# Kernel optimization log

Measured on AMD Instinct MI355X. Metric: run time of the kernel, lower is better.

The kernel has to match this reference:

```python
import jax, jax.numpy as jnp
import numpy as np
from jax import lax


def setup_inputs() -> dict:
    key = jax.random.key(0)
    kx, kw = jax.random.split(key)
    x = jax.random.normal(kx, (8, 32, 16, 160, 160), dtype=jnp.float32)
    # xavier-normal-ish init (scale irrelevant to correctness testing)
    weights = jax.random.normal(kw, (32, 32, 1, 3, 3), dtype=jnp.float32) * 0.1
    return {"x": x, "weights": weights}


def reference(x, weights):
    # per-(out_ch, in_ch) scale: mean |w| over kernel dims (2,3,4), detached
    scale = lax.stop_gradient(jnp.mean(jnp.abs(weights), axis=(2, 3, 4), keepdims=True))
    binary_no_grad = scale * jnp.sign(weights)          # {+-scale}
    clipped = jnp.clip(weights, -1.0, 1.0)
    # straight-through estimator: value = binary_no_grad, grad flows via clipped
    binary_weights = lax.stop_gradient(binary_no_grad - clipped) + clipped
    out = lax.conv_general_dilated(
        x, binary_weights,
        window_strides=(1, 1, 1),
        padding=((0, 0), (1, 1), (1, 1)),
        rhs_dilation=(1, 1, 1),
        dimension_numbers=("NCDHW", "OIDHW", "NCDHW"),
        feature_group_count=1,
    )
    return out
```

## Files before the change

kernel.cpp:

```cpp
#include <hip/hip_runtime.h>
#include <stdint.h>


typedef _Float16 half8  __attribute__((ext_vector_type(8)));
typedef float    floatx4 __attribute__((ext_vector_type(4)));

#define DHW 409600
#define HW  25600
#define RING_SLOT_B 10368
#define RING_B      41472
#define SCR_SLOT_B  20480
#define LDS_TOTAL   102912

__device__ __forceinline__ int w1s(int w1) { return w1 ^ ((w1 >> 2) & 1); }
__device__ __forceinline__ int f2v(int w1) { return ((w1 >> 1) ^ (w1 >> 3)) & 3; }

typedef const __attribute__((address_space(1))) uint32_t* gas1;
typedef __attribute__((address_space(3))) uint32_t* las3;
__device__ __forceinline__ void gld16(const void* g, void* l) {
    __builtin_amdgcn_global_load_lds((gas1)g, (las3)l, 16, 0, 0);
}
#define VMCNT(N) do { asm volatile("s_waitcnt vmcnt(" #N ")" ::: "memory"); \
                      __builtin_amdgcn_sched_barrier(0); } while (0)
__device__ __forceinline__ void barrier_raw() {
    __builtin_amdgcn_sched_barrier(0);
    asm volatile("s_waitcnt lgkmcnt(0)" ::: "memory");
    __builtin_amdgcn_s_barrier();
    __builtin_amdgcn_sched_barrier(0);
}

__global__ void bnn_wprep_kernel(const float* __restrict__ w,
                                 _Float16* __restrict__ ws) {
    const int tid = threadIdx.x;
    #pragma unroll
    for (int p4 = 0; p4 < 4; ++p4) {
        const int oi = tid * 4 + p4;
        const int o  = oi >> 5;
        const int i  = oi & 31;
        const float* wp = w + oi * 9;
        float s = 0.f;
        #pragma unroll
        for (int t = 0; t < 9; ++t) s += fabsf(wp[t]);
        s *= (1.f / 9.f);
        const int l = ((i >> 3) << 4) | (o & 15);
        const int p = o >> 4;
        const int j = i & 7;
        #pragma unroll
        for (int t = 0; t < 9; ++t) {
            const float v  = wp[t];
            const float sg = (v > 0.f) ? 1.f : ((v < 0.f) ? -1.f : 0.f);
            ws[((t * 2 + p) * 64 + l) * 8 + j] = (_Float16)(s * sg);
        }
    }
}

__global__ __launch_bounds__(320) void bnn_conv3d_dma(
        const float* __restrict__ x, const _Float16* __restrict__ ws,
        float* __restrict__ out) {
    extern __shared__ __align__(16) char lds[];

    const int tid  = threadIdx.x;
    const int lane = tid & 63;
    const int wv   = tid >> 6;

    const int bid = blockIdx.x;
    const int hc  = bid & 3;
    const int d   = (bid >> 2) & 15;
    const int n   = bid >> 6;
    const int h0  = hc * 40;

    const float* qb[4];
    {
        const int chl = lane >> 3;
        const int wl  = (lane & 7) * 4;
        #pragma unroll
        for (int q = 0; q < 4; ++q)
            qb[q] = x + (size_t)(n * 32 + q * 8 + chl) * DHW + d * HW + wv * 32 + wl;
    }

    half8 wf0[9], wf1[9];
    {
        const half8* fb = (const half8*)ws;
        #pragma unroll
        for (int t = 0; t < 9; ++t) {
            wf0[t] = fb[(t * 2 + 0) * 64 + lane];
            wf1[t] = fb[(t * 2 + 1) * 64 + lane];
        }
    }
    asm volatile("s_waitcnt vmcnt(0)" ::: "memory");
    __builtin_amdgcn_sched_barrier(0);

    if (tid < 128) {
        const int slot = tid >> 5, w1x = ((tid >> 4) & 1) ? 161 : 0, word = tid & 15;
        *(uint32_t*)(lds + slot * RING_SLOT_B + w1x * 64 + word * 4) = 0u;
    }

    const int pcell = 32 * wv + 1 + (lane >> 1);
    const int w1p   = w1s(pcell);
    const int wloc  = (w1p - 1) - wv * 32;
    const int chb   = (lane & 1) * 16;
    int soff[16];
    #pragma unroll
    for (int c = 0; c < 16; ++c) {
        const int ch = chb + c;
        soff[c] = (wv * 4 + (ch >> 3)) * 1024 + ((ch & 7) * 8 + (wloc >> 2)) * 16
                + (wloc & 3) * 4;
    }
    const int f2p = f2v(pcell);
    const int rb0 = pcell * 64 + ((((lane & 1) * 2)     ^ f2p) * 16);
    const int rb1 = pcell * 64 + ((((lane & 1) * 2 + 1) ^ f2p) * 16);

    const int s16 = lane & 15, kgr = lane >> 4;
    int rdo[2][3];
    #pragma unroll
    for (int gi = 0; gi < 2; ++gi)
        #pragma unroll
        for (int kw = 0; kw < 3; ++kw) {
            const int w1 = (2 * wv + gi) * 16 + s16 + kw;
            rdo[gi][kw] = (w1s(w1) * 32 + ((kgr ^ f2v(w1)) * 8)) * 2;
        }
    float* ob = out + (size_t)(n * 32 + s16) * DHW + d * HW + wv * 32 + kgr * 4;

    auto DMA = [&](int r) {
        int h = h0 - 1 + r; h = h < 0 ? 0 : (h > 159 ? 159 : h);
        char* dst = lds + RING_B + (r % 3) * SCR_SLOT_B + wv * 4096;
        #pragma unroll
        for (int q = 0; q < 4; ++q)
            gld16(qb[q] + h * 160, dst + q * 1024);
        __builtin_amdgcn_sched_barrier(0);
    };
    auto PACK = [&](int r) {
        const int hr = h0 - 1 + r;
        const char* sl = lds + RING_B + (r % 3) * SCR_SLOT_B;
        char* rg = lds + (r & 3) * RING_SLOT_B;
        half8 o0 = {}, o1 = {};
        if (hr >= 0 && hr < 160) {
            float f[16];
            #pragma unroll
            for (int c = 0; c < 16; ++c) f[c] = *(const float*)(sl + soff[c]);
            #pragma unroll
            for (int c = 0; c < 8; ++c) { o0[c] = (_Float16)f[c]; o1[c] = (_Float16)f[c + 8]; }
        }
        *(half8*)(rg + rb0) = o0;
        *(half8*)(rg + rb1) = o1;
    };
    auto COMPUTE = [&](int t) {
        #pragma unroll
        for (int gi = 0; gi < 2; ++gi) {
            floatx4 a0 = {0.f, 0.f, 0.f, 0.f};
            floatx4 a1 = {0.f, 0.f, 0.f, 0.f};
            #pragma unroll
            for (int kh = 0; kh < 3; ++kh) {
                const char* sb = lds + ((t + kh) & 3) * RING_SLOT_B;
                #pragma unroll
                for (int kw = 0; kw < 3; ++kw) {
                    const half8 a = *(const half8*)(sb + rdo[gi][kw]);
                    const int tp = kh * 3 + kw;
                    a0 = __builtin_amdgcn_mfma_f32_16x16x32_f16(a, wf0[tp], a0, 0, 0, 0);
                    a1 = __builtin_amdgcn_mfma_f32_16x16x32_f16(a, wf1[tp], a1, 0, 0, 0);
                }
            }
            float* op = ob + (size_t)(h0 + t) * 160 + gi * 16;
            *(floatx4*)op = a0;
            *(floatx4*)(op + (size_t)16 * DHW) = a1;
        }
    };

    DMA(0); DMA(1); DMA(2);
    VMCNT(8);  PACK(0);
    VMCNT(4);  PACK(1);
    barrier_raw();
    DMA(3);
    VMCNT(4);  PACK(2); barrier_raw(); DMA(4); COMPUTE(0);
    VMCNT(8);  PACK(3); barrier_raw(); DMA(5); COMPUTE(1);
    for (int t = 2; t <= 37; ++t) {
        VMCNT(12); PACK(t + 2); barrier_raw(); DMA(t + 4); COMPUTE(t);
    }
    VMCNT(12); PACK(40); barrier_raw(); COMPUTE(38);
    VMCNT(8);  PACK(41); barrier_raw(); COMPUTE(39);
}

extern "C" void kernel_launch(void* const* d_in, const int* in_sizes, int n_in,
                              void* d_out, int out_size, void* d_ws, size_t ws_size,
                              hipStream_t stream) {
    const float* x = (const float*)d_in[0];
    const float* w = (const float*)d_in[1];
    float* out = (float*)d_out;
    _Float16* ws = (_Float16*)d_ws;
    bnn_wprep_kernel<<<dim3(1), dim3(256), 0, stream>>>(w, ws);
    (void)hipFuncSetAttribute((const void*)&bnn_conv3d_dma,
                              hipFuncAttributeMaxDynamicSharedMemorySize, LDS_TOTAL);
    bnn_conv3d_dma<<<dim3(512), dim3(320), LDS_TOTAL, stream>>>(x, ws, out);
}
```

Before: 188.5 us.

## Drop halo columns and triple staging buffer to fit two blocks per CU

Removes the zero-padded halo cells from the fp16 ring, clamping column reads instead and zeroing the A fragment with a select at the image edges. The fp32 staging scratch goes from three slots to two, and the prologue gets an extra barrier to keep the reuse safe. Together these cut dynamic LDS from about 100 KB to 80 KB, so two blocks can share a CU and hide memory latency better. The cost is a couple of extra selects per compute step and a tighter DMA/pack reuse window.

```diff
diff --git a/kernel.cpp b/kernel.cpp
--- a/kernel.cpp
+++ b/kernel.cpp
@@ -7,10 +7,10 @@
 
 #define DHW 409600
 #define HW  25600
-#define RING_SLOT_B 10368
-#define RING_B      41472
+#define RING_SLOT_B 10240
+#define RING_B      40960
 #define SCR_SLOT_B  20480
-#define LDS_TOTAL   102912
+#define LDS_TOTAL   81920
 
 __device__ __forceinline__ int w1s(int w1) { return w1 ^ ((w1 >> 2) & 1); }
 __device__ __forceinline__ int f2v(int w1) { return ((w1 >> 1) ^ (w1 >> 3)) & 3; }
@@ -90,14 +90,9 @@
     asm volatile("s_waitcnt vmcnt(0)" ::: "memory");
     __builtin_amdgcn_sched_barrier(0);
 
-    if (tid < 128) {
-        const int slot = tid >> 5, w1x = ((tid >> 4) & 1) ? 161 : 0, word = tid & 15;
-        *(uint32_t*)(lds + slot * RING_SLOT_B + w1x * 64 + word * 4) = 0u;
-    }
-
-    const int pcell = 32 * wv + 1 + (lane >> 1);
+    const int pcell = 32 * wv + (lane >> 1);
     const int w1p   = w1s(pcell);
-    const int wloc  = (w1p - 1) - wv * 32;
+    const int wloc  = w1p - wv * 32;
     const int chb   = (lane & 1) * 16;
     int soff[16];
     #pragma unroll
@@ -116,14 +111,17 @@
     for (int gi = 0; gi < 2; ++gi)
         #pragma unroll
         for (int kw = 0; kw < 3; ++kw) {
-            const int w1 = (2 * wv + gi) * 16 + s16 + kw;
-            rdo[gi][kw] = (w1s(w1) * 32 + ((kgr ^ f2v(w1)) * 8)) * 2;
+            int wq = (2 * wv + gi) * 16 + s16 + kw - 1;
+            wq = wq < 0 ? 0 : (wq > 159 ? 159 : wq);
+            rdo[gi][kw] = (w1s(wq) * 32 + ((kgr ^ f2v(wq)) * 8)) * 2;
         }
+    const bool okA = (wv * 32 + s16 - 1) >= 0;
+    const bool okB = (wv * 32 + 16 + s16 + 1) < 160;
     float* ob = out + (size_t)(n * 32 + s16) * DHW + d * HW + wv * 32 + kgr * 4;
 
     auto DMA = [&](int r) {
         int h = h0 - 1 + r; h = h < 0 ? 0 : (h > 159 ? 159 : h);
-        char* dst = lds + RING_B + (r % 3) * SCR_SLOT_B + wv * 4096;
+        char* dst = lds + RING_B + (r & 1) * SCR_SLOT_B + wv * 4096;
         #pragma unroll
         for (int q = 0; q < 4; ++q)
             gld16(qb[q] + h * 160, dst + q * 1024);
@@ -131,7 +129,7 @@
     };
     auto PACK = [&](int r) {
         const int hr = h0 - 1 + r;
-        const char* sl = lds + RING_B + (r % 3) * SCR_SLOT_B;
+        const char* sl = lds + RING_B + (r & 1) * SCR_SLOT_B;
         char* rg = lds + (r & 3) * RING_SLOT_B;
         half8 o0 = {}, o1 = {};
         if (hr >= 0 && hr < 160) {
@@ -145,6 +143,7 @@
         *(half8*)(rg + rb1) = o1;
     };
     auto COMPUTE = [&](int t) {
+        const half8 zh = {};
         #pragma unroll
         for (int gi = 0; gi < 2; ++gi) {
             floatx4 a0 = {0.f, 0.f, 0.f, 0.f};
@@ -154,7 +153,9 @@
                 const char* sb = lds + ((t + kh) & 3) * RING_SLOT_B;
                 #pragma unroll
                 for (int kw = 0; kw < 3; ++kw) {
-                    const half8 a = *(const half8*)(sb + rdo[gi][kw]);
+                    half8 a = *(const half8*)(sb + rdo[gi][kw]);
+                    if (gi == 0 && kw == 0) a = okA ? a : zh;
+                    if (gi == 1 && kw == 2) a = okB ? a : zh;
                     const int tp = kh * 3 + kw;
                     a0 = __builtin_amdgcn_mfma_f32_16x16x32_f16(a, wf0[tp], a0, 0, 0, 0);
                     a1 = __builtin_amdgcn_mfma_f32_16x16x32_f16(a, wf1[tp], a1, 0, 0, 0);
@@ -166,11 +167,11 @@
         }
     };
 
-    DMA(0); DMA(1); DMA(2);
-    VMCNT(8);  PACK(0);
+    DMA(0); DMA(1);
+    VMCNT(4);  PACK(0);
+    barrier_raw(); DMA(2);
     VMCNT(4);  PACK(1);
-    barrier_raw();
-    DMA(3);
+    barrier_raw(); DMA(3);
     VMCNT(4);  PACK(2); barrier_raw(); DMA(4); COMPUTE(0);
     VMCNT(8);  PACK(3); barrier_raw(); DMA(5); COMPUTE(1);
     for (int t = 2; t <= 37; ++t) {
```

After: 188.7 us. About the same (+0.1%).
